# Performance work log

Hardware: AMD Instinct MI355X
Metric: run time of the kernel (lower is better)

Reference implementation:

```python
import jax, jax.numpy as jnp
import numpy as np

D = 1024
H = 16
HS = D // H
DFF = 4 * D
EPS = 1e-5


def setup_inputs() -> dict:
    key = jax.random.key(0)
    ks = jax.random.split(key, 16)
    s_attn = 1.0 / np.sqrt(D)
    x = jax.random.normal(ks[0], (4, 2048, D), dtype=jnp.float32)
    wq = jax.random.normal(ks[1], (H, D, HS), dtype=jnp.float32) * s_attn
    wk = jax.random.normal(ks[2], (H, D, HS), dtype=jnp.float32) * s_attn
    wv = jax.random.normal(ks[3], (H, D, HS), dtype=jnp.float32) * s_attn
    wo = jax.random.normal(ks[4], (D, D), dtype=jnp.float32) * s_attn
    bo = jnp.zeros((D,), dtype=jnp.float32)
    w1 = jax.random.normal(ks[5], (D, DFF), dtype=jnp.float32) * s_attn
    b1 = jnp.zeros((DFF,), dtype=jnp.float32)
    w2 = jax.random.normal(ks[6], (DFF, D), dtype=jnp.float32) * (1.0 / np.sqrt(DFF))
    b2 = jnp.zeros((D,), dtype=jnp.float32)
    g1 = jnp.ones((D,), dtype=jnp.float32)
    be1 = jnp.zeros((D,), dtype=jnp.float32)
    g2 = jnp.ones((D,), dtype=jnp.float32)
    be2 = jnp.zeros((D,), dtype=jnp.float32)
    return {"x": x, "wq": wq, "wk": wk, "wv": wv, "wo": wo, "bo": bo,
            "w1": w1, "b1": b1, "w2": w2, "b2": b2,
            "g1": g1, "be1": be1, "g2": g2, "be2": be2}


def _layernorm(x, g, b):
    mu = jnp.mean(x, axis=-1, keepdims=True)
    var = jnp.mean(jnp.square(x - mu), axis=-1, keepdims=True)
    return (x - mu) * jax.lax.rsqrt(var + EPS) * g + b


def _block(x, wq, wk, wv, wo, bo, w1, b1, w2, b2, g1, be1, g2, be2):
    B, T, C = x.shape
    h = _layernorm(x, g1, be1)
    q = jnp.einsum('btd,hdk->bhtk', h, wq)
    k = jnp.einsum('btd,hdk->bhtk', h, wk)
    v = jnp.einsum('btd,hdk->bhtk', h, wv)
    wei = jnp.einsum('bhtk,bhsk->bhts', q, k) * (HS ** -0.5)
    causal = jnp.tril(jnp.ones((T, T), dtype=bool))
    wei = jnp.where(causal, wei, -jnp.inf)
    wei = jax.nn.softmax(wei, axis=-1)
    attn = jnp.einsum('bhts,bhsk->bhtk', wei, v)  # (B,H,T,HS)
    attn = attn.transpose(0, 2, 1, 3).reshape(B, T, C)  # concat heads
    x = x + attn @ wo + bo
    h2 = _layernorm(x, g2, be2)
    ff = jax.nn.relu(h2 @ w1 + b1) @ w2 + b2
    return x + ff


def reference(x, wq, wk, wv, wo, bo, w1, b1, w2, b2, g1, be1, g2, be2):
    return _block(x, wq, wk, wv, wo, bo, w1, b1, w2, b2, g1, be1, g2, be2)
```

## Files before the change

### kernel.cpp

```cpp
#include <hip/hip_runtime.h>
#include <hip/hip_bf16.h>

#define D_ 1024
#define T_ 2048
#define B_ 4
#define H_ 16
#define HS_ 64
#define DFF_ 4096
#define M_TOT 8192

typedef short s8v __attribute__((ext_vector_type(8)));
typedef float f4v __attribute__((ext_vector_type(4)));

__device__ __forceinline__ void gll16(const void* g, void* l) {
  __builtin_amdgcn_global_load_lds(
      (__attribute__((address_space(1))) void*)(g),
      (__attribute__((address_space(3))) void*)(l), 16, 0, 0);
}

__device__ __forceinline__ short f2b(float f) {
  __hip_bfloat16 h = __float2bfloat16(f);
  short s; __builtin_memcpy(&s, &h, 2); return s;
}

__global__ __launch_bounds__(256) void transpose_all_kernel(
    const float* __restrict__ wq, const float* __restrict__ wk,
    const float* __restrict__ wv, const float* __restrict__ wo,
    const float* __restrict__ w1, const float* __restrict__ w2,
    __hip_bfloat16* __restrict__ qkvT, __hip_bfloat16* __restrict__ woT,
    __hip_bfloat16* __restrict__ w1T, __hip_bfloat16* __restrict__ w2T) {
  const int bid = blockIdx.x;
  const float* src; __hip_bfloat16* dst;
  int R, C, rb, bx, by;
  if (bid < 3072) {
    int j = bid >> 10, w = bid & 1023;
    src = (j == 0) ? wq : (j == 1) ? wk : wv;
    dst = qkvT; R = 1024; C = 64;
    int z = w >> 6, xy = w & 63;
    bx = xy & 1; by = xy >> 1;
    src += (size_t)z * R * C;
    rb = j * 1024 + z * C;
  } else if (bid < 4096) {
    int w = bid - 3072;
    src = wo; dst = woT; R = 1024; C = 1024; rb = 0;
    bx = w & 31; by = w >> 5;
  } else if (bid < 8192) {
    int w = bid - 4096;
    src = w1; dst = w1T; R = 1024; C = 4096; rb = 0;
    bx = w & 127; by = w >> 7;
  } else {
    int w = bid - 8192;
    src = w2; dst = w2T; R = 4096; C = 1024; rb = 0;
    bx = w & 31; by = w >> 5;
  }
  __shared__ float tile[32][33];
  int c0 = bx * 32, r0 = by * 32;
  int tx = threadIdx.x, ty = threadIdx.y;
#pragma unroll
  for (int i = 0; i < 4; ++i)
    tile[ty + i * 8][tx] = src[(size_t)(r0 + ty + i * 8) * C + c0 + tx];
  __syncthreads();
#pragma unroll
  for (int i = 0; i < 4; ++i)
    dst[(size_t)(rb + c0 + ty + i * 8) * R + r0 + tx] =
        __float2bfloat16(tile[tx][ty + i * 8]);
}

__global__ __launch_bounds__(256) void transpose_v_kernel(
    const __hip_bfloat16* __restrict__ Vb, __hip_bfloat16* __restrict__ Vt) {
  const int bh = blockIdx.y;
  const int t0 = blockIdx.x * 64;
  __shared__ short tile[64][72];
  const int tid = threadIdx.x;
  const int r = tid >> 2, cg = tid & 3;
  const __hip_bfloat16* src = Vb + ((size_t)bh * T_ + t0 + r) * HS_ + cg * 16;
  s8v v0 = *(const s8v*)(src);
  s8v v1 = *(const s8v*)(src + 8);
  *(s8v*)&tile[r][cg * 16] = v0;
  *(s8v*)&tile[r][cg * 16 + 8] = v1;
  __syncthreads();
  const int hs = r;
  short o0[8], o1[8];
#pragma unroll
  for (int k2 = 0; k2 < 8; ++k2) o0[k2] = tile[cg * 16 + k2][hs];
#pragma unroll
  for (int k2 = 0; k2 < 8; ++k2) o1[k2] = tile[cg * 16 + 8 + k2][hs];
  __hip_bfloat16* dst = Vt + ((size_t)bh * HS_ + hs) * T_ + t0 + cg * 16;
  *(s8v*)dst = *(s8v*)o0;
  *(s8v*)(dst + 8) = *(s8v*)o1;
}

__global__ __launch_bounds__(256) void ln_kernel(
    const float* __restrict__ x, const float* __restrict__ g,
    const float* __restrict__ be, __hip_bfloat16* __restrict__ out) {
  int row = blockIdx.x;
  int t = threadIdx.x;
  float4 v = ((const float4*)(x + (size_t)row * D_))[t];
  float s = v.x + v.y + v.z + v.w;
  float ss = v.x * v.x + v.y * v.y + v.z * v.z + v.w * v.w;
#pragma unroll
  for (int o = 1; o < 64; o <<= 1) { s += __shfl_xor(s, o); ss += __shfl_xor(ss, o); }
  __shared__ float rs[4], rss[4];
  int w = t >> 6, l = t & 63;
  if (l == 0) { rs[w] = s; rss[w] = ss; }
  __syncthreads();
  s = rs[0] + rs[1] + rs[2] + rs[3];
  ss = rss[0] + rss[1] + rss[2] + rss[3];
  float mu = s * (1.f / D_);
  float var = ss * (1.f / D_) - mu * mu;
  float r = rsqrtf(var + 1e-5f);
  float4 gv = ((const float4*)g)[t];
  float4 bv = ((const float4*)be)[t];
  union { ushort4 u; __hip_bfloat16 h[4]; } pk;
  pk.h[0] = __float2bfloat16((v.x - mu) * r * gv.x + bv.x);
  pk.h[1] = __float2bfloat16((v.y - mu) * r * gv.y + bv.y);
  pk.h[2] = __float2bfloat16((v.z - mu) * r * gv.z + bv.z);
  pk.h[3] = __float2bfloat16((v.w - mu) * r * gv.w + bv.w);
  ((ushort4*)(out + (size_t)row * D_))[t] = pk.u;
}

template <int EPI>
__global__ __launch_bounds__(256) void gemm_bt_kernel(
    const __hip_bfloat16* __restrict__ A, const __hip_bfloat16* __restrict__ Bt,
    int M, int N, int K,
    void* __restrict__ p0, void* __restrict__ p1, void* __restrict__ p2,
    const float* __restrict__ bias, const float* __restrict__ res) {
  __shared__ short sA[2][128 * 32], sB[2][128 * 32];
  const int gdx = gridDim.x;
  const int nwg = gdx * gridDim.y;
  const int orig = blockIdx.y * gdx + blockIdx.x;
  const int xcd = orig & 7;
  const int c = orig >> 3;
  const int rows = (nwg >> 3) / gdx;
  const int i2 = c & 1;
  const int nn = (c >> 1) % gdx;
  const int gg = (c >> 1) / gdx;
  const int mrow = xcd * rows + gg * 2 + i2;
  const int m0 = mrow * 128, n0 = nn * 128;
  const int t = threadIdx.x, l = t & 63, w = t >> 6;
  const int wr = w >> 1, wc = w & 1, lg = l >> 4, lo = l & 15;
  f4v acc[4][4];
#pragma unroll
  for (int m = 0; m < 4; ++m)
#pragma unroll
    for (int n = 0; n < 4; ++n) acc[m][n] = (f4v){0.f, 0.f, 0.f, 0.f};
  const int nkt = K >> 5;
  auto stage = [&](int kt, int bi) {
#pragma unroll
    for (int j = 0; j < 2; ++j) {
      int i = j * 256 + t;
      int row = i >> 2, kc = i & 3;
      gll16(A + (size_t)(m0 + row) * K + kt * 32 + kc * 8, (char*)sA[bi] + i * 16);
      gll16(Bt + (size_t)(n0 + row) * K + kt * 32 + kc * 8, (char*)sB[bi] + i * 16);
    }
  };
  stage(0, 0);
  __syncthreads();
  for (int kt = 0; kt < nkt; ++kt) {
    const int bi = kt & 1;
    if (kt + 1 < nkt) stage(kt + 1, bi ^ 1);
    s8v af[4], bf[4];
#pragma unroll
    for (int m = 0; m < 4; ++m)
      af[m] = *(const s8v*)((const char*)sA[bi] + (wr * 64 + m * 16 + lo) * 64 + lg * 16);
#pragma unroll
    for (int n = 0; n < 4; ++n)
      bf[n] = *(const s8v*)((const char*)sB[bi] + (wc * 64 + n * 16 + lo) * 64 + lg * 16);
#pragma unroll
    for (int m = 0; m < 4; ++m)
#pragma unroll
      for (int n = 0; n < 4; ++n)
        acc[m][n] = __builtin_amdgcn_mfma_f32_16x16x32_bf16(af[m], bf[n], acc[m][n], 0, 0, 0);
    __syncthreads();
  }
#pragma unroll
  for (int mi = 0; mi < 4; ++mi)
#pragma unroll
    for (int j = 0; j < 4; ++j) {
      int mg = m0 + wr * 64 + mi * 16 + lg * 4 + j;
#pragma unroll
      for (int ni = 0; ni < 4; ++ni) {
        int ng = n0 + wc * 64 + ni * 16 + lo;
        float v = acc[mi][ni][j];
        if constexpr (EPI == 0) {
          int wi = ng >> 10, within = ng & 1023, hh = within >> 6, hs = within & 63;
          __hip_bfloat16* dst = (wi == 0) ? (__hip_bfloat16*)p0
                               : (wi == 1) ? (__hip_bfloat16*)p1
                                           : (__hip_bfloat16*)p2;
          int b = mg >> 11, tt = mg & 2047;
          dst[(((size_t)(b * H_ + hh)) * T_ + tt) * HS_ + hs] = __float2bfloat16(v);
        } else if constexpr (EPI == 1) {
          ((float*)p0)[(size_t)mg * N + ng] = res[(size_t)mg * N + ng] + v + bias[ng];
        } else {
          float y = v + bias[ng];
          y = y > 0.f ? y : 0.f;
          ((__hip_bfloat16*)p0)[(size_t)mg * N + ng] = __float2bfloat16(y);
        }
      }
    }
}

template <bool MASK>
__device__ __forceinline__ void attn_step(
    int s0, int qrow, int lg, int lo,
    const short* __restrict__ sKb, const short* __restrict__ sVb,
    short* __restrict__ sPw,
    const s8v (&qf)[2][2], f4v (&acc)[2][4], float (&rsum)[2][4]) {
  s8v kf[4][2];
#pragma unroll
  for (int si = 0; si < 4; ++si) {
    int row = si * 16 + lo;
#pragma unroll
    for (int kc = 0; kc < 2; ++kc) {
      int slot = (kc * 4 + lg) ^ (row & 7);
      kf[si][kc] = *(const s8v*)((const char*)sKb + row * 128 + slot * 16);
    }
  }
  f4v sfr[2][4];
#pragma unroll
  for (int mi = 0; mi < 2; ++mi)
#pragma unroll
    for (int si = 0; si < 4; ++si) {
      sfr[mi][si] = (f4v){0.f, 0.f, 0.f, 0.f};
#pragma unroll
      for (int kc = 0; kc < 2; ++kc)
        sfr[mi][si] = __builtin_amdgcn_mfma_f32_16x16x32_bf16(
            qf[mi][kc], kf[si][kc], sfr[mi][si], 0, 0, 0);
    }
  const float c = 0.18033688f;
  float p[2][4][4];
#pragma unroll
  for (int mi = 0; mi < 2; ++mi)
#pragma unroll
    for (int si = 0; si < 4; ++si)
#pragma unroll
      for (int j = 0; j < 4; ++j) {
        float vv = sfr[mi][si][j] * c;
        if (MASK) {
          int r = qrow + mi * 16 + lg * 4 + j;
          int s = s0 + si * 16 + lo;
          vv = (s <= r) ? vv : -3e38f;
        }
        float e = exp2f(vv);
        p[mi][si][j] = e;
        rsum[mi][j] += e;
      }
#pragma unroll
  for (int mi = 0; mi < 2; ++mi)
#pragma unroll
    for (int si = 0; si < 4; ++si)
#pragma unroll
      for (int j = 0; j < 4; ++j) {
        int row = mi * 16 + lg * 4 + j;
        int s = si * 16 + lo;
        int slot = (s >> 3) ^ (row & 7);
        *(short*)((char*)sPw + row * 128 + slot * 16 + (s & 7) * 2) =
            f2b(p[mi][si][j]);
      }
  s8v pa[2][2], vf[4][2];
#pragma unroll
  for (int mi = 0; mi < 2; ++mi) {
    int row = mi * 16 + lo;
#pragma unroll
    for (int sb = 0; sb < 2; ++sb) {
      int slot = (sb * 4 + lg) ^ (row & 7);
      pa[mi][sb] = *(const s8v*)((const char*)sPw + row * 128 + slot * 16);
    }
  }
#pragma unroll
  for (int ni = 0; ni < 4; ++ni) {
    int row = ni * 16 + lo;
#pragma unroll
    for (int sb = 0; sb < 2; ++sb) {
      int slot = (sb * 4 + lg) ^ (row & 7);
      vf[ni][sb] = *(const s8v*)((const char*)sVb + row * 128 + slot * 16);
    }
  }
#pragma unroll
  for (int mi = 0; mi < 2; ++mi)
#pragma unroll
    for (int ni = 0; ni < 4; ++ni)
#pragma unroll
      for (int sb = 0; sb < 2; ++sb)
        acc[mi][ni] = __builtin_amdgcn_mfma_f32_16x16x32_bf16(
            pa[mi][sb], vf[ni][sb], acc[mi][ni], 0, 0, 0);
}

__global__ __launch_bounds__(256) void attn_kernel(
    const __hip_bfloat16* __restrict__ Q, const __hip_bfloat16* __restrict__ K,
    const __hip_bfloat16* __restrict__ Vt, __hip_bfloat16* __restrict__ O) {
  const int bh = blockIdx.y;
  const int t = threadIdx.x, w = t >> 6, l = t & 63, lg = l >> 4, lo = l & 15;
  const size_t kbase = (size_t)bh * T_ * HS_;
  const size_t vbase = (size_t)bh * HS_ * T_;
  __shared__ short sK[2][64 * 64];
  __shared__ short sV[2][64 * 64];
  __shared__ short sP[4][32 * 64];
  const int b = bh >> 4, hh = bh & 15;
  for (int pass = 0; pass < 2; ++pass) {
    const int tile = pass ? (15 - (int)blockIdx.x) : (int)blockIdx.x;
    const int q0 = tile * 128;
    const int qrow = q0 + w * 32;
    s8v qf[2][2];
#pragma unroll
    for (int mi = 0; mi < 2; ++mi)
#pragma unroll
      for (int kc = 0; kc < 2; ++kc)
        qf[mi][kc] = *(const s8v*)(Q + kbase +
                                   (size_t)(qrow + mi * 16 + lo) * HS_ +
                                   kc * 32 + lg * 8);
    f4v acc[2][4];
    float rsum[2][4];
#pragma unroll
    for (int mi = 0; mi < 2; ++mi) {
#pragma unroll
      for (int ni = 0; ni < 4; ++ni) acc[mi][ni] = (f4v){0.f, 0.f, 0.f, 0.f};
#pragma unroll
      for (int j = 0; j < 4; ++j) rsum[mi][j] = 0.f;
    }
    const int nst = q0 / 64 + 2;
    auto stg = [&](int st) {
      int bi = st & 1;
      int s0 = st * 64;
#pragma unroll
      for (int r = 0; r < 2; ++r) {
        int i = r * 256 + t;
        int row = i >> 3, sl = i & 7;
        int sls = sl ^ (row & 7);
        gll16(K + kbase + (size_t)(s0 + row) * HS_ + sls * 8,
              (char*)sK[bi] + i * 16);
        gll16(Vt + vbase + (size_t)row * T_ + s0 + sls * 8,
              (char*)sV[bi] + i * 16);
      }
    };
    stg(0);
    __syncthreads();
    for (int st = 0; st < nst; ++st) {
      if (st + 1 < nst) stg(st + 1);
      const int s0 = st * 64;
      if (s0 <= qrow + 31) {
        if (st < nst - 2)
          attn_step<false>(s0, qrow, lg, lo, sK[st & 1], sV[st & 1], sP[w],
                           qf, acc, rsum);
        else
          attn_step<true>(s0, qrow, lg, lo, sK[st & 1], sV[st & 1], sP[w],
                          qf, acc, rsum);
      }
      __syncthreads();
    }
#pragma unroll
    for (int mi = 0; mi < 2; ++mi)
#pragma unroll
      for (int j = 0; j < 4; ++j) {
        float rs = rsum[mi][j];
#pragma unroll
        for (int o = 1; o < 16; o <<= 1) rs += __shfl_xor(rs, o);
        int r = qrow + mi * 16 + lg * 4 + j;
        float inv = 1.f / rs;
#pragma unroll
        for (int ni = 0; ni < 4; ++ni) {
          int cc = ni * 16 + lo;
          O[((size_t)b * T_ + r) * D_ + hh * HS_ + cc] =
              __float2bfloat16(acc[mi][ni][j] * inv);
        }
      }
  }
}

extern "C" void kernel_launch(void* const* d_in, const int* in_sizes, int n_in,
                              void* d_out, int out_size, void* d_ws, size_t ws_size,
                              hipStream_t stream) {
  const float* x   = (const float*)d_in[0];
  const float* wq  = (const float*)d_in[1];
  const float* wk  = (const float*)d_in[2];
  const float* wv  = (const float*)d_in[3];
  const float* wo  = (const float*)d_in[4];
  const float* bo  = (const float*)d_in[5];
  const float* w1  = (const float*)d_in[6];
  const float* b1  = (const float*)d_in[7];
  const float* w2  = (const float*)d_in[8];
  const float* b2  = (const float*)d_in[9];
  const float* g1  = (const float*)d_in[10];
  const float* be1 = (const float*)d_in[11];
  const float* g2  = (const float*)d_in[12];
  const float* be2 = (const float*)d_in[13];
  float* out = (float*)d_out;

  char* ws = (char*)d_ws;
  auto alloc = [&](size_t bytes) {
    char* p = ws;
    ws += (bytes + 255) & ~(size_t)255;
    return p;
  };
  __hip_bfloat16* qkvT  = (__hip_bfloat16*)alloc((size_t)3 * D_ * D_ * 2);
  __hip_bfloat16* woT   = (__hip_bfloat16*)alloc((size_t)D_ * D_ * 2);
  __hip_bfloat16* w1T   = (__hip_bfloat16*)alloc((size_t)DFF_ * D_ * 2);
  __hip_bfloat16* w2T   = (__hip_bfloat16*)alloc((size_t)D_ * DFF_ * 2);
  __hip_bfloat16* hbuf  = (__hip_bfloat16*)alloc((size_t)M_TOT * D_ * 2);
  float*          x1    = (float*)alloc((size_t)M_TOT * D_ * 4);
  __hip_bfloat16* Vtb   = (__hip_bfloat16*)x1;
  char* aliased = alloc((size_t)M_TOT * DFF_ * 2);
  __hip_bfloat16* Qb    = (__hip_bfloat16*)(aliased);
  __hip_bfloat16* Kb    = (__hip_bfloat16*)(aliased + (size_t)M_TOT * D_ * 2);
  __hip_bfloat16* Vb    = (__hip_bfloat16*)(aliased + (size_t)M_TOT * D_ * 4);
  __hip_bfloat16* attnb = (__hip_bfloat16*)(aliased + (size_t)M_TOT * D_ * 6);
  __hip_bfloat16* ffb   = (__hip_bfloat16*)(aliased);

  transpose_all_kernel<<<dim3(12288), dim3(32, 8), 0, stream>>>(
      wq, wk, wv, wo, w1, w2, qkvT, woT, w1T, w2T);
  ln_kernel<<<M_TOT, 256, 0, stream>>>(x, g1, be1, hbuf);
  gemm_bt_kernel<0><<<dim3(24, 64), 256, 0, stream>>>(hbuf, qkvT, M_TOT, 3 * D_, D_,
                                                      Qb, Kb, Vb, nullptr, nullptr);
  transpose_v_kernel<<<dim3(32, 64), 256, 0, stream>>>(Vb, Vtb);
  attn_kernel<<<dim3(8, 64), 256, 0, stream>>>(Qb, Kb, Vtb, attnb);
  gemm_bt_kernel<1><<<dim3(8, 64), 256, 0, stream>>>(attnb, woT, M_TOT, D_, D_,
                                                     x1, nullptr, nullptr, bo, x);
  ln_kernel<<<M_TOT, 256, 0, stream>>>(x1, g2, be2, hbuf);
  gemm_bt_kernel<2><<<dim3(32, 64), 256, 0, stream>>>(hbuf, w1T, M_TOT, DFF_, D_,
                                                      ffb, nullptr, nullptr, b1, nullptr);
  gemm_bt_kernel<1><<<dim3(8, 64), 256, 0, stream>>>(ffb, w2T, M_TOT, D_, DFF_,
                                                     out, nullptr, nullptr, b2, x1);
}
```

Before: 520.5 us.

## Add 256x256-tile GEMM with swizzled LDS and deeper prefetch for QKV/FFN1

Adds a new 512-thread GEMM kernel with 256x256 output tiles, used for the wide QKV and FFN-up projections, to raise data reuse per loaded tile. Both GEMM kernels now XOR-swizzle the LDS layout to reduce bank conflicts. They also prefetch two k-steps ahead with explicit vmcnt waits and raw barriers instead of __syncthreads, and raise wave priority around the MFMA blocks. The larger tile increases register pressure, and the grid for QKV drops to fewer workgroups, which can hurt occupancy and balance across CUs.

```diff
diff --git a/kernel.cpp b/kernel.cpp
--- a/kernel.cpp
+++ b/kernel.cpp
@@ -22,6 +22,9 @@
   __hip_bfloat16 h = __float2bfloat16(f);
   short s; __builtin_memcpy(&s, &h, 2); return s;
 }
+
+#define VMCNT(N) asm volatile("s_waitcnt vmcnt(" #N ")" ::: "memory")
+#define SBAR()  do { __builtin_amdgcn_s_barrier(); __builtin_amdgcn_sched_barrier(0); } while (0)
 
 __global__ __launch_bounds__(256) void transpose_all_kernel(
     const float* __restrict__ wq, const float* __restrict__ wk,
@@ -119,12 +122,11 @@
   ((ushort4*)(out + (size_t)row * D_))[t] = pk.u;
 }
 
-template <int EPI>
 __global__ __launch_bounds__(256) void gemm_bt_kernel(
     const __hip_bfloat16* __restrict__ A, const __hip_bfloat16* __restrict__ Bt,
     int M, int N, int K,
-    void* __restrict__ p0, void* __restrict__ p1, void* __restrict__ p2,
-    const float* __restrict__ bias, const float* __restrict__ res) {
+    float* __restrict__ p0, const float* __restrict__ bias,
+    const float* __restrict__ res) {
   __shared__ short sA[2][128 * 32], sB[2][128 * 32];
   const int gdx = gridDim.x;
   const int nwg = gdx * gridDim.y;
@@ -135,8 +137,7 @@
   const int i2 = c & 1;
   const int nn = (c >> 1) % gdx;
   const int gg = (c >> 1) / gdx;
-  const int mrow = xcd * rows + gg * 2 + i2;
-  const int m0 = mrow * 128, n0 = nn * 128;
+  const int m0 = (xcd * rows + gg * 2 + i2) * 128, n0 = nn * 128;
   const int t = threadIdx.x, l = t & 63, w = t >> 6;
   const int wr = w >> 1, wc = w & 1, lg = l >> 4, lo = l & 15;
   f4v acc[4][4];
@@ -144,34 +145,48 @@
   for (int m = 0; m < 4; ++m)
 #pragma unroll
     for (int n = 0; n < 4; ++n) acc[m][n] = (f4v){0.f, 0.f, 0.f, 0.f};
-  const int nkt = K >> 5;
+  const int NT = K >> 5;
   auto stage = [&](int kt, int bi) {
 #pragma unroll
     for (int j = 0; j < 2; ++j) {
       int i = j * 256 + t;
-      int row = i >> 2, kc = i & 3;
-      gll16(A + (size_t)(m0 + row) * K + kt * 32 + kc * 8, (char*)sA[bi] + i * 16);
-      gll16(Bt + (size_t)(n0 + row) * K + kt * 32 + kc * 8, (char*)sB[bi] + i * 16);
+      int row = i >> 2, sl = i & 3;
+      int ss = sl ^ ((row >> 1) & 3);
+      gll16(A + (size_t)(m0 + row) * K + kt * 32 + ss * 8, (char*)sA[bi] + i * 16);
+      gll16(Bt + (size_t)(n0 + row) * K + kt * 32 + ss * 8, (char*)sB[bi] + i * 16);
     }
   };
   stage(0, 0);
-  __syncthreads();
-  for (int kt = 0; kt < nkt; ++kt) {
+  stage(1, 1);
+  VMCNT(4);
+  SBAR();
+  for (int kt = 0; kt < NT; ++kt) {
     const int bi = kt & 1;
-    if (kt + 1 < nkt) stage(kt + 1, bi ^ 1);
     s8v af[4], bf[4];
 #pragma unroll
-    for (int m = 0; m < 4; ++m)
-      af[m] = *(const s8v*)((const char*)sA[bi] + (wr * 64 + m * 16 + lo) * 64 + lg * 16);
-#pragma unroll
-    for (int n = 0; n < 4; ++n)
-      bf[n] = *(const s8v*)((const char*)sB[bi] + (wc * 64 + n * 16 + lo) * 64 + lg * 16);
+    for (int m = 0; m < 4; ++m) {
+      int row = wr * 64 + m * 16 + lo;
+      int ss = lg ^ ((row >> 1) & 3);
+      af[m] = *(const s8v*)((const char*)sA[bi] + row * 64 + ss * 16);
+    }
+#pragma unroll
+    for (int n = 0; n < 4; ++n) {
+      int row = wc * 64 + n * 16 + lo;
+      int ss = lg ^ ((row >> 1) & 3);
+      bf[n] = *(const s8v*)((const char*)sB[bi] + row * 64 + ss * 16);
+    }
+    __builtin_amdgcn_s_setprio(1);
 #pragma unroll
     for (int m = 0; m < 4; ++m)
 #pragma unroll
       for (int n = 0; n < 4; ++n)
         acc[m][n] = __builtin_amdgcn_mfma_f32_16x16x32_bf16(af[m], bf[n], acc[m][n], 0, 0, 0);
-    __syncthreads();
+    __builtin_amdgcn_s_setprio(0);
+    if (kt == NT - 1) break;
+    SBAR();
+    if (kt + 2 < NT) { stage(kt + 2, bi); VMCNT(4); }
+    else             { VMCNT(0); }
+    SBAR();
   }
 #pragma unroll
   for (int mi = 0; mi < 4; ++mi)
@@ -181,6 +196,108 @@
 #pragma unroll
       for (int ni = 0; ni < 4; ++ni) {
         int ng = n0 + wc * 64 + ni * 16 + lo;
+        p0[(size_t)mg * N + ng] = res[(size_t)mg * N + ng] + acc[mi][ni][j] + bias[ng];
+      }
+    }
+}
+
+template <int EPI>
+__global__ __launch_bounds__(512, 2) void gemm_bt_256(
+    const __hip_bfloat16* __restrict__ A, const __hip_bfloat16* __restrict__ Bt,
+    int M, int N, int K,
+    void* __restrict__ p0, void* __restrict__ p1, void* __restrict__ p2,
+    const float* __restrict__ bias) {
+  __shared__ short sA[2][256 * 32], sB[2][256 * 32];
+  const int gdx = gridDim.x;
+  const int gdy = gridDim.y;
+  const int orig = blockIdx.y * gdx + blockIdx.x;
+  const int xcd = orig & 7;
+  const int c = orig >> 3;
+  const int rowsPerXcd = gdy >> 3;
+  const int g = c / (2 * gdx);
+  const int r = c % (2 * gdx);
+  const int i2 = r & 1, nn = r >> 1;
+  const int m0 = (xcd * rowsPerXcd + g * 2 + i2) * 256;
+  const int n0 = nn * 256;
+  const int t = threadIdx.x, l = t & 63, wid = t >> 6;
+  const int wm = wid >> 2, wn = wid & 3, lg = l >> 4, lo = l & 15;
+  f4v acc[8][4];
+#pragma unroll
+  for (int m = 0; m < 8; ++m)
+#pragma unroll
+    for (int n = 0; n < 4; ++n) acc[m][n] = (f4v){0.f, 0.f, 0.f, 0.f};
+  const int NT = K >> 5;
+  auto stage = [&](int kt, int bi) {
+#pragma unroll
+    for (int j = 0; j < 2; ++j) {
+      int i = j * 512 + t;
+      int row = i >> 2, sl = i & 3;
+      int ss = sl ^ ((row >> 1) & 3);
+      gll16(A + (size_t)(m0 + row) * K + kt * 32 + ss * 8, (char*)sA[bi] + i * 16);
+      gll16(Bt + (size_t)(n0 + row) * K + kt * 32 + ss * 8, (char*)sB[bi] + i * 16);
+    }
+  };
+  stage(0, 0);
+  stage(1, 1);
+  VMCNT(4);
+  SBAR();
+  for (int kt = 0; kt < NT; ++kt) {
+    const int bi = kt & 1;
+    const char* cA = (const char*)sA[bi];
+    const char* cB = (const char*)sB[bi];
+    s8v bf[4];
+#pragma unroll
+    for (int nr = 0; nr < 4; ++nr) {
+      int row = wn * 64 + nr * 16 + lo;
+      int ss = lg ^ ((row >> 1) & 3);
+      bf[nr] = *(const s8v*)(cB + row * 64 + ss * 16);
+    }
+    {
+      s8v af[4];
+#pragma unroll
+      for (int mr = 0; mr < 4; ++mr) {
+        int row = wm * 128 + mr * 16 + lo;
+        int ss = lg ^ ((row >> 1) & 3);
+        af[mr] = *(const s8v*)(cA + row * 64 + ss * 16);
+      }
+      __builtin_amdgcn_s_setprio(1);
+#pragma unroll
+      for (int mr = 0; mr < 4; ++mr)
+#pragma unroll
+        for (int nr = 0; nr < 4; ++nr)
+          acc[mr][nr] = __builtin_amdgcn_mfma_f32_16x16x32_bf16(af[mr], bf[nr], acc[mr][nr], 0, 0, 0);
+      __builtin_amdgcn_s_setprio(0);
+    }
+    {
+      s8v af[4];
+#pragma unroll
+      for (int mr = 0; mr < 4; ++mr) {
+        int row = wm * 128 + (mr + 4) * 16 + lo;
+        int ss = lg ^ ((row >> 1) & 3);
+        af[mr] = *(const s8v*)(cA + row * 64 + ss * 16);
+      }
+      __builtin_amdgcn_s_setprio(1);
+#pragma unroll
+      for (int mr = 0; mr < 4; ++mr)
+#pragma unroll
+        for (int nr = 0; nr < 4; ++nr)
+          acc[mr + 4][nr] = __builtin_amdgcn_mfma_f32_16x16x32_bf16(af[mr], bf[nr], acc[mr + 4][nr], 0, 0, 0);
+      __builtin_amdgcn_s_setprio(0);
+    }
+    if (kt == NT - 1) break;
+    SBAR();
+    if (kt + 2 < NT) { stage(kt + 2, bi); VMCNT(4); }
+    else             { VMCNT(0); }
+    SBAR();
+  }
+#pragma unroll
+  for (int mi = 0; mi < 8; ++mi)
+#pragma unroll
+    for (int j = 0; j < 4; ++j) {
+      int mg = m0 + wm * 128 + mi * 16 + lg * 4 + j;
+#pragma unroll
+      for (int ni = 0; ni < 4; ++ni) {
+        int ng = n0 + wn * 64 + ni * 16 + lo;
         float v = acc[mi][ni][j];
         if constexpr (EPI == 0) {
           int wi = ng >> 10, within = ng & 1023, hh = within >> 6, hs = within & 63;
@@ -189,8 +306,6 @@
                                            : (__hip_bfloat16*)p2;
           int b = mg >> 11, tt = mg & 2047;
           dst[(((size_t)(b * H_ + hh)) * T_ + tt) * HS_ + hs] = __float2bfloat16(v);
-        } else if constexpr (EPI == 1) {
-          ((float*)p0)[(size_t)mg * N + ng] = res[(size_t)mg * N + ng] + v + bias[ng];
         } else {
           float y = v + bias[ng];
           y = y > 0.f ? y : 0.f;
@@ -409,15 +524,15 @@
   transpose_all_kernel<<<dim3(12288), dim3(32, 8), 0, stream>>>(
       wq, wk, wv, wo, w1, w2, qkvT, woT, w1T, w2T);
   ln_kernel<<<M_TOT, 256, 0, stream>>>(x, g1, be1, hbuf);
-  gemm_bt_kernel<0><<<dim3(24, 64), 256, 0, stream>>>(hbuf, qkvT, M_TOT, 3 * D_, D_,
-                                                      Qb, Kb, Vb, nullptr, nullptr);
+  gemm_bt_256<0><<<dim3(12, 32), 512, 0, stream>>>(hbuf, qkvT, M_TOT, 3 * D_, D_,
+                                                   Qb, Kb, Vb, nullptr);
   transpose_v_kernel<<<dim3(32, 64), 256, 0, stream>>>(Vb, Vtb);
   attn_kernel<<<dim3(8, 64), 256, 0, stream>>>(Qb, Kb, Vtb, attnb);
-  gemm_bt_kernel<1><<<dim3(8, 64), 256, 0, stream>>>(attnb, woT, M_TOT, D_, D_,
-                                                     x1, nullptr, nullptr, bo, x);
+  gemm_bt_kernel<<<dim3(8, 64), 256, 0, stream>>>(attnb, woT, M_TOT, D_, D_,
+                                                  x1, bo, x);
   ln_kernel<<<M_TOT, 256, 0, stream>>>(x1, g2, be2, hbuf);
-  gemm_bt_kernel<2><<<dim3(32, 64), 256, 0, stream>>>(hbuf, w1T, M_TOT, DFF_, D_,
-                                                      ffb, nullptr, nullptr, b1, nullptr);
-  gemm_bt_kernel<1><<<dim3(8, 64), 256, 0, stream>>>(ffb, w2T, M_TOT, D_, DFF_,
-                                                     out, nullptr, nullptr, b2, x1);
-}
+  gemm_bt_256<2><<<dim3(16, 32), 512, 0, stream>>>(hbuf, w1T, M_TOT, DFF_, D_,
+                                                   ffb, nullptr, nullptr, b1);
+  gemm_bt_kernel<<<dim3(8, 64), 256, 0, stream>>>(ffb, w2T, M_TOT, D_, DFF_,
+                                                  out, b2, x1);
+}
```

Measured after the change: 544.3 us. 1.05x slower.
